# Kernel optimization log

Hardware: AMD Instinct MI355X
Metric: run time of the kernel (lower is better)

Reference implementation:

```python
import jax, jax.numpy as jnp
import numpy as np

B, D, N, WD, R, NW = 1024, 1024, 256, 64, 4, 1
EPS = 1e-6


def _dense(x, W, b):
    return x @ W + b


def _cosine_weights(memory, keys, strengths):
    # memory [B,N,WD], keys [B,K,WD], strengths [B,K] -> softmax cosine weights [B,K,N]
    dot = jnp.einsum('bkw,bnw->bkn', keys, memory)
    mn = jnp.linalg.norm(memory, axis=-1)  # [B,N]
    kn = jnp.linalg.norm(keys, axis=-1)    # [B,K]
    sim = dot / (kn[:, :, None] * mn[:, None, :] + EPS)
    return jax.nn.softmax(sim * strengths[:, :, None], axis=-1)


def _allocation(usage):
    # DNC Freeness allocation: sort by non-usage, exclusive cumprod of usage, unsort.
    usage = EPS + (1.0 - EPS) * usage
    nonusage = 1.0 - usage
    idx = jnp.argsort(-nonusage, axis=-1)            # descending non-usage
    s_non = jnp.take_along_axis(nonusage, idx, axis=-1)
    s_use = 1.0 - s_non
    cp = jnp.cumprod(s_use, axis=-1)
    excl = jnp.concatenate([jnp.ones_like(cp[:, :1]), cp[:, :-1]], axis=-1)
    s_alloc = s_non * excl
    inv = jnp.argsort(idx, axis=-1)                  # inverse permutation
    return jnp.take_along_axis(s_alloc, inv, axis=-1)


def _forward(controller, memory, prev_read_weights, prev_write_weights, prev_link,
             prev_precedence, prev_usage, params):
    (W_wv, b_wv, W_ev, b_ev, W_fg, b_fg, W_ag, b_ag, W_wg, b_wg,
     W_rm, b_rm, W_ws, b_ws, W_rs, b_rs, W_wk, b_wk, W_rk, b_rk) = params
    Bsz = controller.shape[0]

    # _read_inputs: small dense projections of controller output
    write_vectors = _dense(controller, W_wv, b_wv).reshape(Bsz, NW, WD)
    erase_vectors = jax.nn.sigmoid(_dense(controller, W_ev, b_ev)).reshape(Bsz, NW, WD)
    free_gate = jax.nn.sigmoid(_dense(controller, W_fg, b_fg))          # [B,R]
    allocation_gate = jax.nn.sigmoid(_dense(controller, W_ag, b_ag))    # [B,NW]
    write_gate = jax.nn.sigmoid(_dense(controller, W_wg, b_wg))         # [B,NW]
    read_mode = jax.nn.softmax(_dense(controller, W_rm, b_rm).reshape(Bsz, R, 1 + 2 * NW), axis=-1)
    write_keys = _dense(controller, W_wk, b_wk).reshape(Bsz, NW, WD)
    write_strengths = jax.nn.softplus(_dense(controller, W_ws, b_ws))   # [B,NW]
    read_keys = _dense(controller, W_rk, b_rk).reshape(Bsz, R, WD)
    read_strengths = jax.nn.softplus(_dense(controller, W_rs, b_rs))    # [B,R]

    # Freeness: usage update (not differentiable wrt write weights, per DNC)
    ww_sg = jax.lax.stop_gradient(prev_write_weights)
    agg_ww = 1.0 - jnp.prod(1.0 - ww_sg, axis=1)                        # [B,N]
    usage_after_write = prev_usage + (1.0 - prev_usage) * agg_ww
    phi = jnp.prod(1.0 - free_gate[:, :, None] * prev_read_weights, axis=1)
    usage = usage_after_write * phi

    # write weights: content + allocation mixed by gates
    write_content = _cosine_weights(memory, write_keys, write_strengths)  # [B,NW,N]
    write_gates = allocation_gate * write_gate
    alloc_list = []
    u = usage
    for i in range(NW):
        a = _allocation(u)
        alloc_list.append(a)
        u = u + (1.0 - u) * write_gates[:, i:i + 1] * a
    write_alloc = jnp.stack(alloc_list, axis=1)                           # [B,NW,N]
    ag = allocation_gate[:, :, None]
    wg = write_gate[:, :, None]
    write_weights = wg * (ag * write_alloc + (1.0 - ag) * write_content)

    # erase and write
    weighted_resets = write_weights[:, :, :, None] * erase_vectors[:, :, None, :]  # [B,NW,N,WD]
    reset_gate = jnp.prod(1.0 - weighted_resets, axis=1)                           # [B,N,WD]
    memory = memory * reset_gate + jnp.einsum('bwn,bwd->bnd', write_weights, write_vectors)

    # temporal linkage update
    ww_i = write_weights[:, :, :, None]
    ww_j = write_weights[:, :, None, :]
    new_link = ww_i * prev_precedence[:, :, None, :]
    link = (1.0 - ww_i - ww_j) * prev_link + new_link
    link = link * (1.0 - jnp.eye(N, dtype=link.dtype))                   # zero diagonal
    precedence = (1.0 - jnp.sum(write_weights, axis=-1, keepdims=True)) * prev_precedence + write_weights

    # read weights: content + directional (forward/backward over link)
    read_content = _cosine_weights(memory, read_keys, read_strengths)    # [B,R,N]
    forward_w = jnp.einsum('brn,bwmn->brwm', prev_read_weights, link)    # adjoint_b=True
    backward_w = jnp.einsum('brn,bwnm->brwm', prev_read_weights, link)
    backward_mode = read_mode[:, :, :NW]
    forward_mode = read_mode[:, :, NW:2 * NW]
    content_mode = read_mode[:, :, 2 * NW]
    read_weights = (content_mode[:, :, None] * read_content
                    + jnp.einsum('brw,brwn->brn', forward_mode, forward_w)
                    + jnp.einsum('brw,brwn->brn', backward_mode, backward_w))
    read_words = jnp.einsum('brn,bnd->brd', read_weights, memory)        # [B,R,WD]
    return read_words, memory, read_weights, write_weights, link, precedence, usage


def setup_inputs() -> dict:
    key = jax.random.key(0)
    ks = jax.random.split(key, 32)
    inp = {
        'controller': jax.random.normal(ks[0], (B, D), jnp.float32),
        'memory': jax.random.normal(ks[1], (B, N, WD), jnp.float32),
        'prev_read_weights': jax.random.uniform(ks[2], (B, R, N), jnp.float32) / N,
        'prev_write_weights': jax.random.uniform(ks[3], (B, NW, N), jnp.float32) / N,
        'prev_link': jnp.zeros((B, NW, N, N), jnp.float32),
        'prev_precedence': jax.random.uniform(ks[4], (B, NW, N), jnp.float32) / N,
        'prev_usage': jax.random.uniform(ks[5], (B, N), jnp.float32),
    }
    dims = [('wv', NW * WD), ('ev', NW * WD), ('fg', R), ('ag', NW), ('wg', NW),
            ('rm', R * (1 + 2 * NW)), ('ws', NW), ('rs', R), ('wk', NW * WD), ('rk', R * WD)]
    i = 6
    for name, od in dims:
        inp['W_' + name] = jax.random.normal(ks[i], (D, od), jnp.float32) * 0.02
        inp['b_' + name] = jnp.zeros((od,), jnp.float32)
        i += 1
    return inp


def reference(controller, memory, prev_read_weights, prev_write_weights, prev_link,
              prev_precedence, prev_usage,
              W_wv, b_wv, W_ev, b_ev, W_fg, b_fg, W_ag, b_ag, W_wg, b_wg,
              W_rm, b_rm, W_ws, b_ws, W_rs, b_rs, W_wk, b_wk, W_rk, b_rk):
    params = (W_wv, b_wv, W_ev, b_ev, W_fg, b_fg, W_ag, b_ag, W_wg, b_wg,
              W_rm, b_rm, W_ws, b_ws, W_rs, b_rs, W_wk, b_wk, W_rk, b_rk)
    return _forward(controller, memory, prev_read_weights, prev_write_weights,
                    prev_link, prev_precedence, prev_usage, params)
```

## Files before the change

kernel.cpp:

```cpp
#include <hip/hip_runtime.h>
#include <math.h>

typedef unsigned short ush;
typedef float v4f __attribute__((ext_vector_type(4)));

#define EPSc 1e-6f

#define NB 1024
#define ND 1024
#define NN 256
#define NWD 64
#define NR 4

#define OFF_RWORDS   ((size_t)0)
#define OFF_MEM      ((size_t)262144)
#define OFF_RWEIGHTS ((size_t)17039360)
#define OFF_WW       ((size_t)18087936)
#define OFF_LINK     ((size_t)18350080)
#define OFF_PREC     ((size_t)85458944)
#define OFF_USAGE    ((size_t)85721088)

#define WS_PART   ((size_t)0)
#define WS_PARAMS ((size_t)2097152)
#define WS_FW     ((size_t)2785280)

struct Ptrs {
  const float* W[10];
  const float* Bv[10];
};

__device__ __forceinline__ float b2f(ush h){
  union { unsigned int u; float f; } v; v.u = ((unsigned int)h) << 16; return v.f;
}
__device__ __forceinline__ ush f2b(float f){
  union { float f; unsigned int u; } v; v.f = f;
  unsigned int u = v.u;
  u += 0x7fffu + ((u >> 16) & 1u);
  return (ush)(u >> 16);
}
__device__ __forceinline__ float u16lo(unsigned int w){
  union { unsigned int u; float f; } v; v.u = w << 16; return v.f;
}
__device__ __forceinline__ float u16hi(unsigned int w){
  union { unsigned int u; float f; } v; v.u = w & 0xffff0000u; return v.f;
}
__device__ __forceinline__ float sigm(float x){ return 1.f/(1.f+expf(-x)); }
__device__ __forceinline__ float softplus(float x){ return fmaxf(x,0.f) + log1pf(expf(-fabsf(x))); }

__device__ __forceinline__ int colmap(int c, int& lc, int& od){
  const int starts[11] = {0,64,128,132,133,134,146,147,151,215,471};
  const int ods[10]    = {64,64,4,1,1,12,1,4,64,256};
  int m = 0;
  #pragma unroll
  for (int i=1;i<10;i++) if (c >= starts[i]) m = i;
  lc = c - starts[m]; od = ods[m];
  return m;
}

__global__ __launch_bounds__(256) void k1_gemm(const float* __restrict__ ctrl, Ptrs P,
                                               float* __restrict__ part){
  int bt = blockIdx.x;
  int kc = blockIdx.y;
  int t  = threadIdx.x;
  int c0 = t;
  bool has1 = (t + 256 < 471);
  int c1 = has1 ? t + 256 : 470;
  int lc0, od0, lc1, od1;
  int m0 = colmap(c0, lc0, od0);
  int m1 = colmap(c1, lc1, od1);
  const float* w0p = P.W[m0] + lc0;
  const float* w1p = P.W[m1] + lc1;
  float acc0[8], acc1[8];
  #pragma unroll
  for (int r=0;r<8;r++){ acc0[r]=0.f; acc1[r]=0.f; }
  const float* cb = ctrl + (size_t)(bt*8)*ND + kc*256;
  for (int d0 = 0; d0 < 256; d0 += 4){
    float4 cv[8];
    #pragma unroll
    for (int r=0;r<8;r++) cv[r] = *(const float4*)(cb + (size_t)r*ND + d0);
    #pragma unroll
    for (int k=0;k<4;k++){
      size_t dg = (size_t)(kc*256 + d0 + k);
      float wv0 = w0p[dg*od0];
      float wv1 = w1p[dg*od1];
      #pragma unroll
      for (int r=0;r<8;r++){
        float cvk = ((const float*)&cv[r])[k];
        acc0[r] += cvk*wv0;
        acc1[r] += cvk*wv1;
      }
    }
  }
  #pragma unroll
  for (int r=0;r<8;r++)
    part[((size_t)kc*NB + bt*8+r)*512 + c0] = acc0[r];
  if (has1){
    #pragma unroll
    for (int r=0;r<8;r++)
      part[((size_t)kc*NB + bt*8+r)*512 + c1] = acc1[r];
  }
}


#define SSTAGE(j,k) { \
  float kp = __shfl_xor(key, (j)); int ip = __shfl_xor(idx, (j)); \
  bool gt = (key > kp) || (key == kp && idx > ip); \
  bool selmin = (((t & (k)) == 0) == ((t & (j)) == 0)); \
  if (selmin == gt){ key = kp; idx = ip; } }

#define LSTAGE(j,k) { \
  sk[t] = key; si[t] = idx; __syncthreads(); \
  float kp = sk[t^(j)]; int ip = si[t^(j)]; \
  bool gt = (key > kp) || (key == kp && idx > ip); \
  bool selmin = (((t & (k)) == 0) == ((t & (j)) == 0)); \
  if (selmin == gt){ key = kp; idx = ip; } \
  __syncthreads(); }

__global__ __launch_bounds__(256) void k2_gates(
    const float* __restrict__ part, Ptrs P,
    const float* __restrict__ mem, const float* __restrict__ prw_in,
    const float* __restrict__ pww_in, const float* __restrict__ pprec,
    const float* __restrict__ pusage,
    float* __restrict__ params,
    float* __restrict__ out_ww, float* __restrict__ out_prec, float* __restrict__ out_usage)
{
  int b = blockIdx.x, t = threadIdx.x;
  int w = t >> 6, l = t & 63;
  __shared__ float proj[512];
  __shared__ float wkL[64];
  __shared__ float scal[12];
  __shared__ float wred[16];
  __shared__ float sk[256];
  __shared__ int   si[256];
  __shared__ float salloc[256];

  for (int c = t; c < 471; c += 256){
    float v = 0.f;
    #pragma unroll
    for (int kc=0;kc<4;kc++) v += part[((size_t)kc*NB + b)*512 + c];
    int lc, od; int m = colmap(c, lc, od);
    v += P.Bv[m][lc];
    proj[c] = v;
  }
  __syncthreads();

  float* pb = params + (size_t)b*672;
  if (t < 64){
    pb[t] = proj[t];
    pb[64+t] = sigm(proj[64+t]);
    wkL[t] = proj[151+t];
  }
  pb[128 + t] = proj[215 + t];
  if (t < 4){
    pb[384 + t] = softplus(proj[147 + t]);
    float a = proj[134 + 3*t], bq = proj[134 + 3*t + 1], c2 = proj[134 + 3*t + 2];
    float mx = fmaxf(a, fmaxf(bq, c2));
    float ea = expf(a-mx), eb = expf(bq-mx), ec = expf(c2-mx);
    float s = ea+eb+ec;
    pb[388 + 3*t]     = ea/s;
    pb[388 + 3*t + 1] = eb/s;
    pb[388 + 3*t + 2] = ec/s;
    scal[t] = sigm(proj[128+t]);
  }
  if (t == 0){
    scal[4] = sigm(proj[132]);
    scal[5] = sigm(proj[133]);
    scal[6] = softplus(proj[146]);
  }
  if (w == 0){
    float kv = proj[151 + l];
    float s2 = kv*kv;
    #pragma unroll
    for (int off=32; off>0; off>>=1) s2 += __shfl_xor(s2, off);
    if (l == 0) scal[7] = sqrtf(s2);
  }
  __syncthreads();

  float us;
  {
    float pu = pusage[(size_t)b*NN + t];
    float pw = pww_in[(size_t)b*NN + t];
    float uaw = pu + (1.f-pu)*pw;
    float phi = 1.f;
    #pragma unroll
    for (int r=0;r<4;r++)
      phi *= (1.f - scal[r]*prw_in[((size_t)b*NR + r)*NN + t]);
    us = uaw*phi;
    out_usage[(size_t)b*NN + t] = us;
  }

  float sim;
  {
    const float* mrow = mem + ((size_t)b*NN + t)*NWD;
    float dot = 0.f, n2 = 0.f;
    for (int d0=0; d0<64; d0+=4){
      float4 q = *(const float4*)(mrow + d0);
      dot += wkL[d0]*q.x + wkL[d0+1]*q.y + wkL[d0+2]*q.z + wkL[d0+3]*q.w;
      n2  += q.x*q.x + q.y*q.y + q.z*q.z + q.w*q.w;
    }
    sim = scal[6]*dot/(scal[7]*sqrtf(n2) + EPSc);
  }
  {
    float m_ = sim;
    #pragma unroll
    for (int off=32; off>0; off>>=1) m_ = fmaxf(m_, __shfl_xor(m_, off));
    if (l == 0) wred[w] = m_;
  }
  __syncthreads();
  float mx = fmaxf(fmaxf(wred[0],wred[1]), fmaxf(wred[2],wred[3]));
  float e = expf(sim - mx);
  {
    float s_ = e;
    #pragma unroll
    for (int off=32; off>0; off>>=1) s_ += __shfl_xor(s_, off);
    if (l == 0) wred[4+w] = s_;
  }
  __syncthreads();
  float content = e / (wred[4]+wred[5]+wred[6]+wred[7]);

  float key = EPSc + (1.f-EPSc)*us;
  int idx = t;
  SSTAGE(1,2)
  SSTAGE(2,4)  SSTAGE(1,4)
  SSTAGE(4,8)  SSTAGE(2,8)  SSTAGE(1,8)
  SSTAGE(8,16) SSTAGE(4,16) SSTAGE(2,16) SSTAGE(1,16)
  SSTAGE(16,32) SSTAGE(8,32) SSTAGE(4,32) SSTAGE(2,32) SSTAGE(1,32)
  SSTAGE(32,64) SSTAGE(16,64) SSTAGE(8,64) SSTAGE(4,64) SSTAGE(2,64) SSTAGE(1,64)
  LSTAGE(64,128)
  SSTAGE(32,128) SSTAGE(16,128) SSTAGE(8,128) SSTAGE(4,128) SSTAGE(2,128) SSTAGE(1,128)
  LSTAGE(128,256)
  LSTAGE(64,256)
  SSTAGE(32,256) SSTAGE(16,256) SSTAGE(8,256) SSTAGE(4,256) SSTAGE(2,256) SSTAGE(1,256)

  float v = key;
  #pragma unroll
  for (int off=1; off<64; off<<=1){
    float u = __shfl_up(v, off);
    if (l >= off) v *= u;
  }
  if (l == 63) wred[8+w] = v;
  __syncthreads();
  float pre = 1.f;
  #pragma unroll
  for (int q=0; q<3; q++) if (q < w) pre *= wred[8+q];
  float exv = __shfl_up(v, 1);
  if (l == 0) exv = 1.f;
  float excl = exv * pre;
  float s_alloc = (1.f - key) * excl;
  salloc[idx] = s_alloc;
  __syncthreads();
  float alloc = salloc[t];

  float ag = scal[4], wg = scal[5];
  float ww = wg*(ag*alloc + (1.f-ag)*content);
  pb[400 + t] = ww;
  out_ww[(size_t)b*NN + t] = ww;
  {
    float s_ = ww;
    #pragma unroll
    for (int off=32; off>0; off>>=1) s_ += __shfl_xor(s_, off);
    if (l == 0) wred[12+w] = s_;
  }
  __syncthreads();
  float wsum = wred[12]+wred[13]+wred[14]+wred[15];
  float prec = (1.f - wsum)*pprec[(size_t)b*NN + t] + ww;
  out_prec[(size_t)b*NN + t] = prec;
}

__global__ __launch_bounds__(256) void k4_link(
    const float* __restrict__ plink, const float* __restrict__ pprec,
    const float* __restrict__ prw_in, const float* __restrict__ params,
    float* __restrict__ out_link, float* __restrict__ fw, float* __restrict__ bwp)
{
  int b = blockIdx.x, cc = blockIdx.y, t = threadIdx.x;
  int w = t >> 6, l = t & 63;
  __shared__ float wwl[256], ppl[256], prwl[4*256];
  __shared__ v4f   bred[4][4][64];
  __shared__ float fwbuf[4*128];
  const float* pb = params + (size_t)b*672;
  wwl[t] = pb[400 + t];
  ppl[t] = pprec[(size_t)b*NN + t];
  #pragma unroll
  for (int r=0;r<4;r++) prwl[r*256 + t] = prw_in[((size_t)b*NR + r)*NN + t];
  __syncthreads();

  v4f wwj = *(const v4f*)&wwl[4*l];
  v4f ppj = *(const v4f*)&ppl[4*l];
  v4f pr0 = *(const v4f*)&prwl[0*256 + 4*l];
  v4f pr1 = *(const v4f*)&prwl[1*256 + 4*l];
  v4f pr2 = *(const v4f*)&prwl[2*256 + 4*l];
  v4f pr3 = *(const v4f*)&prwl[3*256 + 4*l];

  v4f bacc0 = {0.f,0.f,0.f,0.f}, bacc1 = bacc0, bacc2 = bacc0, bacc3 = bacc0;

  int i0 = cc*128 + w*32;
  const v4f* plrow = (const v4f*)(plink + ((size_t)b*NN + i0)*NN) + l;
  float*     olbase = out_link + ((size_t)b*NN + i0)*NN + 4*l;

  #pragma unroll 2
  for (int k=0; k<32; k++){
    int i = i0 + k;
    v4f pl = plrow[(size_t)k*64];
    float wwi = wwl[i];
    float c1  = 1.f - wwi;
    float pi0 = prwl[0*256+i], pi1 = prwl[1*256+i],
          pi2 = prwl[2*256+i], pi3 = prwl[3*256+i];
    v4f lv = (c1 - wwj)*pl + wwi*ppj;
    if (l == (i>>2)) lv[i&3] = 0.f;
    __builtin_nontemporal_store(lv, (v4f*)(olbase + (size_t)k*NN));

    v4f f0 = pr0*lv, f1 = pr1*lv, f2 = pr2*lv, f3 = pr3*lv;
    float s0 = f0.x+f0.y+f0.z+f0.w;
    float s1 = f1.x+f1.y+f1.z+f1.w;
    float s2 = f2.x+f2.y+f2.z+f2.w;
    float s3 = f3.x+f3.y+f3.z+f3.w;
    bacc0 += pi0*lv; bacc1 += pi1*lv; bacc2 += pi2*lv; bacc3 += pi3*lv;

    s0 += __shfl_xor(s0,1); s0 += __shfl_xor(s0,2);
    s1 += __shfl_xor(s1,1); s1 += __shfl_xor(s1,2);
    s2 += __shfl_xor(s2,1); s2 += __shfl_xor(s2,2);
    s3 += __shfl_xor(s3,1); s3 += __shfl_xor(s3,2);
    float v = (l&1) ? ((l&2)? s3 : s1) : ((l&2)? s2 : s0);
    v += __shfl_xor(v,4); v += __shfl_xor(v,8);
    v += __shfl_xor(v,16); v += __shfl_xor(v,32);
    if (l < 4) fwbuf[w*128 + l*32 + k] = v;
  }

  bred[w][0][l] = bacc0;
  bred[w][1][l] = bacc1;
  bred[w][2][l] = bacc2;
  bred[w][3][l] = bacc3;
  __syncthreads();

  {
    int r = t >> 6, l2 = t & 63;
    v4f a = bred[0][r][l2], b4 = bred[1][r][l2],
        c4 = bred[2][r][l2], d4 = bred[3][r][l2];
    v4f s = a + b4 + c4 + d4;
    *(v4f*)&bwp[(((size_t)cc*NB + b)*NR + r)*NN + 4*l2] = s;
    #pragma unroll
    for (int e=0;e<2;e++){
      int idx = t + e*256;
      int rr = idx >> 7, j = idx & 127;
      fw[((size_t)b*NR + rr)*NN + cc*128 + j] = fwbuf[(j>>5)*128 + rr*32 + (j&31)];
    }
  }
}

#define MSTR 264
__global__ __launch_bounds__(256) void k5_read(
    const float* __restrict__ mem, const float* __restrict__ params,
    const float* __restrict__ fw, const float* __restrict__ bwp,
    float* __restrict__ out_rwords, float* __restrict__ out_mem, float* __restrict__ out_rweights)
{
  int b = blockIdx.x, t = threadIdx.x;
  __shared__ ush   memt[64*MSTR];
  __shared__ float wvl[64], erl[64], rkl[256];
  __shared__ float siml[4*260];
  __shared__ float rwl[4*260];
  __shared__ float scal[32];
  const float* pb = params + (size_t)b*672;
  if (t < 64){ wvl[t] = pb[t]; erl[t] = pb[64+t]; }
  rkl[t] = pb[128 + t];
  if (t < 4)  scal[12+t] = pb[384+t];
  if (t < 12) scal[16+t] = pb[388+t];
  __syncthreads();
  if (t < 4){
    float s = 0.f;
    for (int d=0;d<64;d++){ float v = rkl[t*64+d]; s += v*v; }
    scal[t] = sqrtf(s);
  }
  __syncthreads();

  float wwn = pb[400 + t];
  const float* mrow = mem + ((size_t)b*NN + t)*NWD;
  float* orow = out_mem + ((size_t)b*NN + t)*NWD;
  float n2=0.f, dot0=0.f, dot1=0.f, dot2=0.f, dot3=0.f;
  for (int d0=0; d0<64; d0+=4){
    float4 q = *(const float4*)(mrow + d0);
    float4 qo;
    float* qi = (float*)&q;
    float* po = (float*)&qo;
    #pragma unroll
    for (int k=0;k<4;k++){
      int d = d0+k;
      float m = qi[k];
      float nv = m*(1.f - wwn*erl[d]) + wwn*wvl[d];
      po[k] = nv;
      n2 += nv*nv;
      dot0 += rkl[0*64+d]*nv;
      dot1 += rkl[1*64+d]*nv;
      dot2 += rkl[2*64+d]*nv;
      dot3 += rkl[3*64+d]*nv;
      memt[d*MSTR + t] = f2b(nv);
    }
    *(float4*)(orow + d0) = qo;
  }
  float sn = sqrtf(n2);
  siml[0*260+t] = scal[12]*dot0/(scal[0]*sn + EPSc);
  siml[1*260+t] = scal[13]*dot1/(scal[1]*sn + EPSc);
  siml[2*260+t] = scal[14]*dot2/(scal[2]*sn + EPSc);
  siml[3*260+t] = scal[15]*dot3/(scal[3]*sn + EPSc);
  __syncthreads();

  int rr = t >> 6, lane = t & 63;
  {
    float m1 = -1e30f;
    #pragma unroll
    for (int q2=0;q2<4;q2++) m1 = fmaxf(m1, siml[rr*260 + q2*64 + lane]);
    #pragma unroll
    for (int off=32; off>0; off>>=1) m1 = fmaxf(m1, __shfl_xor(m1, off));
    float s1 = 0.f;
    #pragma unroll
    for (int q2=0;q2<4;q2++) s1 += expf(siml[rr*260 + q2*64 + lane] - m1);
    #pragma unroll
    for (int off=32; off>0; off>>=1) s1 += __shfl_xor(s1, off);
    if (lane == 0){ scal[4+rr] = m1; scal[8+rr] = s1; }
  }
  __syncthreads();

  #pragma unroll
  for (int r=0;r<4;r++){
    float c = expf(siml[r*260+t] - scal[4+r]) / scal[8+r];
    float fwv = fw[((size_t)b*NR + r)*NN + t];
    float bwv = bwp[((size_t)b*NR + r)*NN + t]
              + bwp[((size_t)(NB + b)*NR + r)*NN + t];
    float rwv = scal[16+3*r+2]*c + scal[16+3*r+1]*fwv + scal[16+3*r+0]*bwv;
    rwl[r*260 + t] = rwv;
    out_rweights[((size_t)b*NR + r)*NN + t] = rwv;
  }
  __syncthreads();

  {
    float acc = 0.f;
    const ush* mcol = &memt[lane*MSTR];
    const float* rrow = &rwl[rr*260];
    #pragma unroll 4
    for (int q=0; q<32; q++){
      uint4  u  = *(const uint4*)(mcol + 8*q);
      float4 ra = *(const float4*)(rrow + 8*q);
      float4 rb = *(const float4*)(rrow + 8*q + 4);
      acc += ra.x*u16lo(u.x) + ra.y*u16hi(u.x)
           + ra.z*u16lo(u.y) + ra.w*u16hi(u.y)
           + rb.x*u16lo(u.z) + rb.y*u16hi(u.z)
           + rb.z*u16lo(u.w) + rb.w*u16hi(u.w);
    }
    out_rwords[((size_t)b*NR + rr)*NWD + lane] = acc;
  }
}

extern "C" void kernel_launch(void* const* d_in, const int* in_sizes, int n_in,
                              void* d_out, int out_size, void* d_ws, size_t ws_size,
                              hipStream_t stream) {
  const float* ctrl   = (const float*)d_in[0];
  const float* mem    = (const float*)d_in[1];
  const float* prw    = (const float*)d_in[2];
  const float* pww    = (const float*)d_in[3];
  const float* plink  = (const float*)d_in[4];
  const float* pprec  = (const float*)d_in[5];
  const float* pusage = (const float*)d_in[6];
  Ptrs P;
  for (int i=0;i<10;i++){
    P.W[i]  = (const float*)d_in[7 + 2*i];
    P.Bv[i] = (const float*)d_in[8 + 2*i];
  }
  float* ws = (float*)d_ws;
  float* part   = ws + WS_PART;
  float* params = ws + WS_PARAMS;
  float* fw     = ws + WS_FW;

  float* o = (float*)d_out;
  float* out_rwords   = o + OFF_RWORDS;
  float* out_mem      = o + OFF_MEM;
  float* out_rweights = o + OFF_RWEIGHTS;
  float* out_ww       = o + OFF_WW;
  float* out_link     = o + OFF_LINK;
  float* out_prec     = o + OFF_PREC;
  float* out_usage    = o + OFF_USAGE;

  k1_gemm<<<dim3(128,4), 256, 0, stream>>>(ctrl, P, part);
  k2_gates<<<NB, 256, 0, stream>>>(part, P, mem, prw, pww, pprec, pusage,
                                   params, out_ww, out_prec, out_usage);
  k4_link<<<dim3(NB,2), 256, 0, stream>>>(plink, pprec, prw, params, out_link, fw, part);
  k5_read<<<NB, 256, 0, stream>>>(mem, params, fw, part,
                                  out_rwords, out_mem, out_rweights);
}
```

Measured before the change: 778.2 us.

## Stage controller tile in LDS and change bf16 memory staging layout in read kernel

The projection GEMM kernel now cooperatively loads its 8x256 controller tile into shared memory once, instead of each thread re-reading it from global memory. The read kernel stores the updated memory rows in bf16 in row-major form with packed 32-bit writes, replacing the transposed per-element scatter. The final read-word reduction now walks N with scalar LDS loads. The unroll pragma on the link-update loop is removed. The scalar final loop gives up the vectorized 128-bit LDS reads the old code used.

Result: faster. 734.9 us (-5.6%).

```diff
diff --git a/kernel.cpp b/kernel.cpp
--- a/kernel.cpp
+++ b/kernel.cpp
@@ -38,12 +38,6 @@
   u += 0x7fffu + ((u >> 16) & 1u);
   return (ush)(u >> 16);
 }
-__device__ __forceinline__ float u16lo(unsigned int w){
-  union { unsigned int u; float f; } v; v.u = w << 16; return v.f;
-}
-__device__ __forceinline__ float u16hi(unsigned int w){
-  union { unsigned int u; float f; } v; v.u = w & 0xffff0000u; return v.f;
-}
 __device__ __forceinline__ float sigm(float x){ return 1.f/(1.f+expf(-x)); }
 __device__ __forceinline__ float softplus(float x){ return fmaxf(x,0.f) + log1pf(expf(-fabsf(x))); }
 
@@ -62,6 +56,15 @@
   int bt = blockIdx.x;
   int kc = blockIdx.y;
   int t  = threadIdx.x;
+  __shared__ float cl[8*264];
+  #pragma unroll
+  for (int e=0;e<2;e++){
+    int v = t + e*256;
+    int row = v >> 6, chunk = v & 63;
+    const float* src = ctrl + (size_t)(bt*8+row)*ND + kc*256 + chunk*4;
+    *(float4*)&cl[row*264 + chunk*4] = *(const float4*)src;
+  }
+  __syncthreads();
   int c0 = t;
   bool has1 = (t + 256 < 471);
   int c1 = has1 ? t + 256 : 470;
@@ -73,11 +76,10 @@
   float acc0[8], acc1[8];
   #pragma unroll
   for (int r=0;r<8;r++){ acc0[r]=0.f; acc1[r]=0.f; }
-  const float* cb = ctrl + (size_t)(bt*8)*ND + kc*256;
   for (int d0 = 0; d0 < 256; d0 += 4){
-    float4 cv[8];
-    #pragma unroll
-    for (int r=0;r<8;r++) cv[r] = *(const float4*)(cb + (size_t)r*ND + d0);
+    float4 cr[8];
+    #pragma unroll
+    for (int r=0;r<8;r++) cr[r] = *(const float4*)&cl[r*264 + d0];
     #pragma unroll
     for (int k=0;k<4;k++){
       size_t dg = (size_t)(kc*256 + d0 + k);
@@ -85,7 +87,7 @@
       float wv1 = w1p[dg*od1];
       #pragma unroll
       for (int r=0;r<8;r++){
-        float cvk = ((const float*)&cv[r])[k];
+        float cvk = ((const float*)&cr[r])[k];
         acc0[r] += cvk*wv0;
         acc1[r] += cvk*wv1;
       }
@@ -297,7 +299,6 @@
   const v4f* plrow = (const v4f*)(plink + ((size_t)b*NN + i0)*NN) + l;
   float*     olbase = out_link + ((size_t)b*NN + i0)*NN + 4*l;
 
-  #pragma unroll 2
   for (int k=0; k<32; k++){
     int i = i0 + k;
     v4f pl = plrow[(size_t)k*64];
@@ -347,14 +348,13 @@
   }
 }
 
-#define MSTR 264
 __global__ __launch_bounds__(256) void k5_read(
     const float* __restrict__ mem, const float* __restrict__ params,
     const float* __restrict__ fw, const float* __restrict__ bwp,
     float* __restrict__ out_rwords, float* __restrict__ out_mem, float* __restrict__ out_rweights)
 {
   int b = blockIdx.x, t = threadIdx.x;
-  __shared__ ush   memt[64*MSTR];
+  __shared__ ush   memn[256*66];
   __shared__ float wvl[64], erl[64], rkl[256];
   __shared__ float siml[4*260];
   __shared__ float rwl[4*260];
@@ -392,8 +392,11 @@
       dot1 += rkl[1*64+d]*nv;
       dot2 += rkl[2*64+d]*nv;
       dot3 += rkl[3*64+d]*nv;
-      memt[d*MSTR + t] = f2b(nv);
     }
+    unsigned int p01 = (unsigned int)f2b(po[0]) | ((unsigned int)f2b(po[1]) << 16);
+    unsigned int p23 = (unsigned int)f2b(po[2]) | ((unsigned int)f2b(po[3]) << 16);
+    *(unsigned int*)&memn[t*66 + d0]     = p01;
+    *(unsigned int*)&memn[t*66 + d0 + 2] = p23;
     *(float4*)(orow + d0) = qo;
   }
   float sn = sqrtf(n2);
@@ -433,18 +436,7 @@
 
   {
     float acc = 0.f;
-    const ush* mcol = &memt[lane*MSTR];
-    const float* rrow = &rwl[rr*260];
-    #pragma unroll 4
-    for (int q=0; q<32; q++){
-      uint4  u  = *(const uint4*)(mcol + 8*q);
-      float4 ra = *(const float4*)(rrow + 8*q);
-      float4 rb = *(const float4*)(rrow + 8*q + 4);
-      acc += ra.x*u16lo(u.x) + ra.y*u16hi(u.x)
-           + ra.z*u16lo(u.y) + ra.w*u16hi(u.y)
-           + rb.x*u16lo(u.z) + rb.y*u16hi(u.z)
-           + rb.z*u16lo(u.w) + rb.w*u16hi(u.w);
-    }
+    for (int n=0;n<256;n++) acc += rwl[rr*260 + n]*b2f(memn[n*66 + lane]);
     out_rwords[((size_t)b*NR + rr)*NWD + lane] = acc;
   }
 }
```
